# Kernel tuning notes

Measured on AMD Instinct MI355X. Metric: run time of the kernel, lower is better.

Reference implementation:

```python
import jax, jax.numpy as jnp
import numpy as np

EMBED_DIM = 1152
NUM_HEADS = 16
HEAD_DIM = EMBED_DIM // NUM_HEADS  # 72
TOTAL_TOKENS = 4096


def setup_inputs() -> dict:
    key = jax.random.key(0)
    k_x, k_wqkv, k_bqkv, k_wout, k_bout = jax.random.split(key, 5)
    hidden_states = jax.random.normal(k_x, (1, TOTAL_TOKENS, EMBED_DIM), dtype=jnp.float32)
    # fused QKV projection (use_qkv_parallel=True): weight [3*E, E], bias [3*E]
    w_qkv = jax.random.normal(k_wqkv, (3 * EMBED_DIM, EMBED_DIM), dtype=jnp.float32) * 0.02
    b_qkv = jax.random.normal(k_bqkv, (3 * EMBED_DIM,), dtype=jnp.float32) * 0.02
    # output projection [E, E]
    w_out = jax.random.normal(k_wout, (EMBED_DIM, EMBED_DIM), dtype=jnp.float32) * 0.02
    b_out = jax.random.normal(k_bout, (EMBED_DIM,), dtype=jnp.float32) * 0.02
    # 8 ragged sequences packed to 4096 tokens total
    cu_seqlens = jnp.array([0, 300, 900, 1500, 2124, 2600, 3100, 3624, 4096], dtype=jnp.int32)
    return {
        "hidden_states": hidden_states,
        "w_qkv": w_qkv,
        "b_qkv": b_qkv,
        "w_out": w_out,
        "b_out": b_out,
        "cu_seqlens": cu_seqlens,
        "max_seqlen": 1024,
    }


def _varlen_attention(x, w_qkv, b_qkv, w_out, b_out, cu_seqlens):
    # x: [T, E] packed tokens
    T = x.shape[0]
    qkv = x @ w_qkv.T + b_qkv                         # [T, 3E]
    q, k, v = jnp.split(qkv, 3, axis=-1)
    q = q.reshape(T, NUM_HEADS, HEAD_DIM)
    k = k.reshape(T, NUM_HEADS, HEAD_DIM)
    v = v.reshape(T, NUM_HEADS, HEAD_DIM)
    scale = HEAD_DIM ** -0.5
    # block-diagonal (per-sequence) attention via segment-id mask
    seg = jnp.searchsorted(cu_seqlens[1:], jnp.arange(T, dtype=jnp.int32), side="right")
    same_seq = seg[:, None] == seg[None, :]           # [T, T] bool
    scores = jnp.einsum("thd,shd->hts", q, k) * scale  # [H, T, T]
    scores = jnp.where(same_seq[None, :, :], scores, jnp.float32(-1e30))
    attn = jax.nn.softmax(scores, axis=-1)
    out = jnp.einsum("hts,shd->thd", attn, v).reshape(T, EMBED_DIM)
    return out @ w_out.T + b_out                      # [T, E]


def reference(hidden_states, w_qkv, b_qkv, w_out, b_out, cu_seqlens, max_seqlen):
    # max_seqlen is unused by the module (VisionAttention computes internally)
    out = _varlen_attention(hidden_states[0], w_qkv, b_qkv, w_out, b_out, cu_seqlens)
    return out[None]  # (1, total_tokens, embed_dim)
```

## Files before the change

### kernel.cpp

```cpp
#include <hip/hip_runtime.h>
#include <hip/hip_bf16.h>
#include <stdint.h>

typedef __hip_bfloat16 bf16;
typedef __attribute__((ext_vector_type(8))) short short8;
typedef __attribute__((ext_vector_type(4))) float float4v;

#define MFMA16(a, b, c) __builtin_amdgcn_mfma_f32_16x16x32_bf16((a), (b), (c), 0, 0, 0)

static __device__ __forceinline__ short f2bf(float f) {
    bf16 h = __float2bfloat16(f);
    return *reinterpret_cast<short*>(&h);
}

static __device__ __forceinline__ void gl2lds16(const void* g, void* l) {
    __builtin_amdgcn_global_load_lds(
        (const __attribute__((address_space(1))) void*)g,
        (__attribute__((address_space(3))) void*)l, 16, 0, 0);
}

__global__ __launch_bounds__(256) void cvt_all(
    const float* __restrict__ a, bf16* __restrict__ A, int na,
    const float* __restrict__ b, bf16* __restrict__ B, int nb,
    const float* __restrict__ c, bf16* __restrict__ C, int nc,
    float* __restrict__ z, int nz)
{
    int i = (blockIdx.x * 256 + threadIdx.x) * 8;
    const float* src; bf16* dst;
    if (i < na)                 { src = a; dst = A; }
    else if (i < na + nb)       { i -= na; src = b; dst = B; }
    else if (i < na + nb + nc)  { i -= na + nb; src = c; dst = C; }
    else {
        i -= na + nb + nc;
        if (i < nz) {
            const float4v zf = {0.f, 0.f, 0.f, 0.f};
            *(float4v*)(z + i) = zf;
            *(float4v*)(z + i + 4) = zf;
        }
        return;
    }
    const float4v x0 = *(const float4v*)(src + i);
    const float4v x1 = *(const float4v*)(src + i + 4);
    short8 v;
#pragma unroll
    for (int q = 0; q < 4; ++q) { v[q] = f2bf(x0[q]); v[q + 4] = f2bf(x1[q]); }
    *(short8*)(dst + i) = v;
}

__global__ __launch_bounds__(256) void gemm_xwt(
    const bf16* __restrict__ X, const bf16* __restrict__ W,
    const float* __restrict__ bias,
    float* __restrict__ Cout,
    bf16* __restrict__ Qh, bf16* __restrict__ Kh, bf16* __restrict__ Vt,
    int M, int N, int K, int mode)
{
    __shared__ __align__(16) bf16 SMEM[16384];
    bf16* As = SMEM;
    bf16* Bs = SMEM + 8192;

    const int tid  = threadIdx.x;
    const int wave = tid >> 6;
    const int lane = tid & 63;
    const int quad = lane >> 4;
    const int l16  = lane & 15;
    const int m0 = blockIdx.x * 128;
    const int n0 = blockIdx.y * 128;
    const int wm = (wave >> 1) * 64;
    const int wn = (wave & 1) * 64;

    const int lrow   = lane >> 2;
    const int lchunk = lane & 3;

    const int kper = K / gridDim.z;
    const int kbeg = blockIdx.z * kper;
    const int nIt  = kper >> 5;

    float4v acc[4][4];
    const float4v zf = {0.f, 0.f, 0.f, 0.f};
#pragma unroll
    for (int i = 0; i < 4; ++i)
#pragma unroll
        for (int j = 0; j < 4; ++j) acc[i][j] = zf;

    auto stage = [&](int buf, int k0) {
#pragma unroll
        for (int ii = 0; ii < 2; ++ii) {
            const int rbase = wave * 32 + ii * 16;
            const int r  = rbase + lrow;
            const int sc = lchunk ^ ((r >> 1) & 3);
            gl2lds16(&X[(size_t)(m0 + r) * K + k0 + sc * 8], &As[buf * 4096 + rbase * 32]);
            gl2lds16(&W[(size_t)(n0 + r) * K + k0 + sc * 8], &Bs[buf * 4096 + rbase * 32]);
        }
    };

    stage(0, kbeg);

    for (int it = 0; it < nIt; ++it) {
        __syncthreads();
        if (it + 1 < nIt) stage((it + 1) & 1, kbeg + (it + 1) * 32);

        const int b = it & 1;
        short8 af[4], bfr[4];
#pragma unroll
        for (int i = 0; i < 4; ++i) {
            const int r = wm + i * 16 + l16;
            af[i] = *(const short8*)&As[b * 4096 + r * 32 + (quad ^ ((r >> 1) & 3)) * 8];
        }
#pragma unroll
        for (int j = 0; j < 4; ++j) {
            const int r = wn + j * 16 + l16;
            bfr[j] = *(const short8*)&Bs[b * 4096 + r * 32 + (quad ^ ((r >> 1) & 3)) * 8];
        }
#pragma unroll
        for (int i = 0; i < 4; ++i)
#pragma unroll
            for (int j = 0; j < 4; ++j)
                acc[i][j] = MFMA16(af[i], bfr[j], acc[i][j]);
    }

    if (mode == 1 && n0 >= 2304) {
        bf16* T = SMEM;
#pragma unroll 1
        for (int half = 0; half < 2; ++half) {
            __syncthreads();
            if ((wave & 1) == half) {
#pragma unroll
                for (int j = 0; j < 4; ++j) {
                    const int col = n0 + wn + j * 16 + l16;
                    const float bb = bias[col];
#pragma unroll
                    for (int i = 0; i < 4; ++i)
#pragma unroll
                        for (int r = 0; r < 4; ++r)
                            T[(j * 16 + l16) * 136 + wm + i * 16 + quad * 4 + r] =
                                __float2bfloat16(acc[i][j][r] + bb);
                }
            }
            __syncthreads();
            const int dd   = tid >> 2;
            const int tok0 = (tid & 3) * 32;
            const int colg = n0 + half * 64 + dd - 2304;
            const int hh   = colg / 72;
            const int dm   = colg - hh * 72;
            bf16* dst = &Vt[((size_t)hh * 72 + dm) * 4096 + m0 + tok0];
#pragma unroll
            for (int k = 0; k < 4; ++k)
                *(short8*)(dst + k * 8) = *(const short8*)&T[dd * 136 + tok0 + k * 8];
        }
        return;
    }

    const bool split = (gridDim.z > 1);
    const float bscale = (!split || blockIdx.z == 0) ? 1.f : 0.f;
#pragma unroll
    for (int j = 0; j < 4; ++j) {
        const int col = n0 + wn + j * 16 + l16;
        const float bb = bias[col] * bscale;
#pragma unroll
        for (int i = 0; i < 4; ++i) {
#pragma unroll
            for (int r = 0; r < 4; ++r) {
                const int row = m0 + wm + i * 16 + quad * 4 + r;
                const float val = acc[i][j][r] + bb;
                if (mode == 0) {
                    if (split) atomicAdd(&Cout[(size_t)row * N + col], val);
                    else       Cout[(size_t)row * N + col] = val;
                } else {
                    const bf16 bv = __float2bfloat16(val);
                    if (col < 1152) {
                        const int hh = col / 72, dd = col - hh * 72;
                        Qh[((size_t)hh * 4096 + row) * 72 + dd] = bv;
                    } else {
                        const int c2 = col - 1152;
                        const int hh = c2 / 72, dd = c2 - hh * 72;
                        Kh[((size_t)hh * 4096 + row) * 72 + dd] = bv;
                    }
                }
            }
        }
    }
}

__global__ __launch_bounds__(256) void attn_varlen(
    const bf16* __restrict__ Qh, const bf16* __restrict__ Kh,
    const bf16* __restrict__ Vt,
    const int* __restrict__ cu, bf16* __restrict__ AO)
{
    const float scale = 0.11785113019775793f;
    __shared__ __align__(16) bf16 Ks[2][64 * 72];
    __shared__ __align__(16) bf16 Vs[2][80 * 64];
    __shared__ __align__(16) bf16 Ps[4][16 * 72];

    const int tid  = threadIdx.x;
    const int wave = tid >> 6;
    const int lane = tid & 63;
    const int quad = lane >> 4;
    const int l16  = lane & 15;
    const int h  = blockIdx.x & 15;
    const int qb = blockIdx.x >> 4;

    int seq_end = 0, q0 = -1, accb = 0, seq_start = 0;
    for (int i = 0; i < 8; ++i) {
        const int st = cu[i], en = cu[i + 1];
        const int nb = (en - st + 63) >> 6;
        if (q0 < 0 && qb < accb + nb) {
            seq_start = st; seq_end = en; q0 = st + (qb - accb) * 64;
        }
        accb += nb;
    }
    if (q0 < 0) return;

    const bf16 onev  = __float2bfloat16(1.0f);
    const bf16 zerov = __float2bfloat16(0.0f);
    for (int t = tid; t < 1024; t += 256) {
        const int b = t >> 9, rr = (t >> 6) & 7, cc = t & 63;
        Vs[b][(72 + rr) * 64 + cc] = (rr == 0) ? onev : zerov;
    }

    const short8 z8 = {0, 0, 0, 0, 0, 0, 0, 0};

    int qrow_f = q0 + wave * 16 + l16; if (qrow_f > 4095) qrow_f = 4095;
    const bf16* qp = &Qh[((size_t)h * 4096 + qrow_f) * 72];
    short8 aq[3];
    aq[0] = *(const short8*)(qp + quad * 8);
    aq[1] = *(const short8*)(qp + 32 + quad * 8);
    aq[2] = (quad == 0) ? *(const short8*)(qp + 64) : z8;

    const bf16* kbase = &Kh[(size_t)h * 4096 * 72];
    auto stage = [&](int buf, int kv0) {
        const bf16* ksrc = kbase + (size_t)kv0 * 72;
        for (int i = wave; i < 9; i += 4)
            gl2lds16(ksrc + i * 512 + lane * 8, &Ks[buf][i * 512]);
        for (int i = wave; i < 9; i += 4) {
            const int d  = i * 8 + (lane >> 3);
            const int ch = (lane & 7) ^ (d & 7);
            gl2lds16(&Vt[((size_t)h * 72 + d) * 4096 + kv0 + ch * 8],
                     &Vs[buf][i * 512]);
        }
    };

    const float4v zf = {0.f, 0.f, 0.f, 0.f};
    float4v oacc[5];
#pragma unroll
    for (int d = 0; d < 5; ++d) oacc[d] = zf;

    const int kvbeg = seq_start & ~63;
    stage(0, kvbeg);

    for (int kv0 = kvbeg; kv0 < seq_end; kv0 += 64) {
        const int b = ((kv0 - kvbeg) >> 6) & 1;
        __syncthreads();
        if (kv0 + 64 < seq_end) stage(b ^ 1, kv0 + 64);

        float4v sc[4];
#pragma unroll
        for (int nt = 0; nt < 4; ++nt) {
            const bf16* kb = &Ks[b][(nt * 16 + l16) * 72];
            float4v s = zf;
            s = MFMA16(aq[0], *(const short8*)(kb + quad * 8), s);
            s = MFMA16(aq[1], *(const short8*)(kb + 32 + quad * 8), s);
            s = MFMA16(aq[2], (quad == 0) ? *(const short8*)(kb + 64) : z8, s);
            sc[nt] = s;
        }

#pragma unroll
        for (int nt = 0; nt < 4; ++nt) {
            const int kv = kv0 + nt * 16 + l16;
            const bool ok = (kv >= seq_start) && (kv < seq_end);
#pragma unroll
            for (int r = 0; r < 4; ++r) {
                const float p = ok ? __expf(sc[nt][r] * scale) : 0.f;
                Ps[wave][(quad * 4 + r) * 72 + nt * 16 + l16] = __float2bfloat16(p);
            }
        }

        const short8 ap0 = *(const short8*)&Ps[wave][l16 * 72 + quad * 8];
        const short8 ap1 = *(const short8*)&Ps[wave][l16 * 72 + 32 + quad * 8];

#pragma unroll
        for (int dt = 0; dt < 5; ++dt) {
            const int vr = dt * 16 + l16;
            const bf16* vb = &Vs[b][vr * 64];
            const short8 bv0 = *(const short8*)(vb + ((quad ^ (vr & 7)) * 8));
            const short8 bv1 = *(const short8*)(vb + (((quad + 4) ^ (vr & 7)) * 8));
            oacc[dt] = MFMA16(ap0, bv0, oacc[dt]);
            oacc[dt] = MFMA16(ap1, bv1, oacc[dt]);
        }
    }

#pragma unroll
    for (int r = 0; r < 4; ++r) {
        const int qrow = q0 + wave * 16 + quad * 4 + r;
        const float lv = __shfl(oacc[4][r], (lane & 48) | 8);
        if (qrow < seq_end) {
            const float inv = (lv > 0.f) ? (1.0f / lv) : 0.f;
#pragma unroll
            for (int d = 0; d < 5; ++d) {
                const int dim = d * 16 + l16;
                if (dim < 72)
                    AO[(size_t)qrow * 1152 + h * 72 + dim] =
                        __float2bfloat16(oacc[d][r] * inv);
            }
        }
    }
}

extern "C" void kernel_launch(void* const* d_in, const int* in_sizes, int n_in,
                              void* d_out, int out_size, void* d_ws, size_t ws_size,
                              hipStream_t stream)
{
    const float* Xf   = (const float*)d_in[0];
    const float* Wqkv = (const float*)d_in[1];
    const float* Bqkv = (const float*)d_in[2];
    const float* Wout = (const float*)d_in[3];
    const float* Bout = (const float*)d_in[4];
    const int*   cu   = (const int*)d_in[5];

    const size_t X16_B  = (size_t)4096 * 1152 * 2;
    const size_t WQ16_B = (size_t)3456 * 1152 * 2;
    const size_t WO16_B = (size_t)1152 * 1152 * 2;
    const size_t H_B    = (size_t)16 * 4096 * 72 * 2;

    char* ws = (char*)d_ws;
    bf16* X16  = (bf16*)ws;
    bf16* WQ16 = (bf16*)(ws + X16_B);
    bf16* WO16 = (bf16*)(ws + X16_B + WQ16_B);
    bf16* Qh   = (bf16*)(ws + X16_B + WQ16_B + WO16_B);
    bf16* Kh   = (bf16*)(ws + X16_B + WQ16_B + WO16_B + H_B);
    bf16* Vt   = (bf16*)(ws + X16_B + WQ16_B + WO16_B + 2 * H_B);
    bf16* AO   = (bf16*)(ws + X16_B + WQ16_B + WO16_B + 3 * H_B);
    float* Out = (float*)d_out;

    dim3 blk(256);
    cvt_all<<<dim3(7200), blk, 0, stream>>>(Xf, X16, 4096 * 1152,
                                            Wqkv, WQ16, 3456 * 1152,
                                            Wout, WO16, 1152 * 1152,
                                            Out, 4096 * 1152);

    gemm_xwt<<<dim3(32, 27, 1), blk, 0, stream>>>(X16, WQ16, Bqkv, nullptr,
                                                  Qh, Kh, Vt, 4096, 3456, 1152, 1);
    attn_varlen<<<dim3(72 * 16), blk, 0, stream>>>(Qh, Kh, Vt, cu, AO);
    gemm_xwt<<<dim3(32, 9, 2), blk, 0, stream>>>(AO, WO16, Bout, Out,
                                                 nullptr, nullptr, nullptr,
                                                 4096, 1152, 1152, 0);
}
```

Before: 231.4 us.

## Drop split-K atomics and output zeroing; stage Q/K epilogue through LDS

The output projection no longer uses split-K with fp32 atomicAdd into a pre-zeroed buffer. It now runs as a dedicated 128x64-tile GEMM that writes results directly, so the conversion kernel no longer has to zero the output. The Q/K epilogue of the QKV GEMM now goes through LDS and writes coalesced 16-byte vectors into the per-head layouts instead of scattered 2-byte stores. These changes cut atomic traffic, a full-size memset and uncoalesced writes, at the cost of an extra LDS round trip and more blocks per output-GEMM tile.

```diff
diff --git a/kernel.cpp b/kernel.cpp
--- a/kernel.cpp
+++ b/kernel.cpp
@@ -22,23 +22,13 @@
 __global__ __launch_bounds__(256) void cvt_all(
     const float* __restrict__ a, bf16* __restrict__ A, int na,
     const float* __restrict__ b, bf16* __restrict__ B, int nb,
-    const float* __restrict__ c, bf16* __restrict__ C, int nc,
-    float* __restrict__ z, int nz)
+    const float* __restrict__ c, bf16* __restrict__ C, int nc)
 {
     int i = (blockIdx.x * 256 + threadIdx.x) * 8;
     const float* src; bf16* dst;
     if (i < na)                 { src = a; dst = A; }
     else if (i < na + nb)       { i -= na; src = b; dst = B; }
-    else if (i < na + nb + nc)  { i -= na + nb; src = c; dst = C; }
-    else {
-        i -= na + nb + nc;
-        if (i < nz) {
-            const float4v zf = {0.f, 0.f, 0.f, 0.f};
-            *(float4v*)(z + i) = zf;
-            *(float4v*)(z + i + 4) = zf;
-        }
-        return;
-    }
+    else                        { i -= na + nb; src = c; dst = C; if (i >= nc) return; }
     const float4v x0 = *(const float4v*)(src + i);
     const float4v x1 = *(const float4v*)(src + i + 4);
     short8 v;
@@ -47,12 +37,11 @@
     *(short8*)(dst + i) = v;
 }
 
-__global__ __launch_bounds__(256) void gemm_xwt(
+__global__ __launch_bounds__(256) void gemm_qkv(
     const bf16* __restrict__ X, const bf16* __restrict__ W,
     const float* __restrict__ bias,
-    float* __restrict__ Cout,
     bf16* __restrict__ Qh, bf16* __restrict__ Kh, bf16* __restrict__ Vt,
-    int M, int N, int K, int mode)
+    int M, int K)
 {
     __shared__ __align__(16) bf16 SMEM[16384];
     bf16* As = SMEM;
@@ -71,9 +60,7 @@
     const int lrow   = lane >> 2;
     const int lchunk = lane & 3;
 
-    const int kper = K / gridDim.z;
-    const int kbeg = blockIdx.z * kper;
-    const int nIt  = kper >> 5;
+    const int nIt = K >> 5;
 
     float4v acc[4][4];
     const float4v zf = {0.f, 0.f, 0.f, 0.f};
@@ -93,11 +80,11 @@
         }
     };
 
-    stage(0, kbeg);
+    stage(0, 0);
 
     for (int it = 0; it < nIt; ++it) {
         __syncthreads();
-        if (it + 1 < nIt) stage((it + 1) & 1, kbeg + (it + 1) * 32);
+        if (it + 1 < nIt) stage((it + 1) & 1, (it + 1) * 32);
 
         const int b = it & 1;
         short8 af[4], bfr[4];
@@ -118,8 +105,9 @@
                 acc[i][j] = MFMA16(af[i], bfr[j], acc[i][j]);
     }
 
-    if (mode == 1 && n0 >= 2304) {
-        bf16* T = SMEM;
+    bf16* T = SMEM;
+
+    if (n0 >= 2304) {
 #pragma unroll 1
         for (int half = 0; half < 2; ++half) {
             __syncthreads();
@@ -150,32 +138,120 @@
         return;
     }
 
-    const bool split = (gridDim.z > 1);
-    const float bscale = (!split || blockIdx.z == 0) ? 1.f : 0.f;
-#pragma unroll
-    for (int j = 0; j < 4; ++j) {
+#pragma unroll 1
+    for (int half = 0; half < 2; ++half) {
+        __syncthreads();
+        if ((wave >> 1) == half) {
+#pragma unroll
+            for (int j = 0; j < 4; ++j) {
+                const int col = n0 + wn + j * 16 + l16;
+                const float bb = bias[col];
+#pragma unroll
+                for (int i = 0; i < 4; ++i)
+#pragma unroll
+                    for (int r = 0; r < 4; ++r)
+                        T[(i * 16 + quad * 4 + r) * 136 + wn + j * 16 + l16] =
+                            __float2bfloat16(acc[i][j][r] + bb);
+            }
+        }
+        __syncthreads();
+        const int rloc = tid >> 2;
+        const int row  = m0 + half * 64 + rloc;
+        const int c0   = (tid & 3) * 32;
+#pragma unroll
+        for (int k = 0; k < 4; ++k) {
+            const int colg = n0 + c0 + k * 8;
+            const bool isQ = (colg < 1152);
+            const int cc = isQ ? colg : colg - 1152;
+            const int hh = cc / 72;
+            const int dd = cc - hh * 72;
+            bf16* dst = (isQ ? Qh : Kh) + ((size_t)hh * 4096 + row) * 72 + dd;
+            *(short8*)dst = *(const short8*)&T[rloc * 136 + c0 + k * 8];
+        }
+    }
+}
+
+__global__ __launch_bounds__(256) void gemm_out(
+    const bf16* __restrict__ X, const bf16* __restrict__ W,
+    const float* __restrict__ bias, float* __restrict__ Cout,
+    int M, int N, int K)
+{
+    __shared__ __align__(16) bf16 As[2][128 * 32];
+    __shared__ __align__(16) bf16 Bs[2][64 * 32];
+
+    const int tid  = threadIdx.x;
+    const int wave = tid >> 6;
+    const int lane = tid & 63;
+    const int quad = lane >> 4;
+    const int l16  = lane & 15;
+    const int m0 = blockIdx.x * 128;
+    const int n0 = blockIdx.y * 64;
+    const int wm = (wave >> 1) * 64;
+    const int wn = (wave & 1) * 32;
+
+    const int lrow   = lane >> 2;
+    const int lchunk = lane & 3;
+
+    const int nIt = K >> 5;
+
+    float4v acc[4][2];
+    const float4v zf = {0.f, 0.f, 0.f, 0.f};
+#pragma unroll
+    for (int i = 0; i < 4; ++i)
+#pragma unroll
+        for (int j = 0; j < 2; ++j) acc[i][j] = zf;
+
+    auto stage = [&](int buf, int k0) {
+#pragma unroll
+        for (int ii = 0; ii < 2; ++ii) {
+            const int rbase = wave * 32 + ii * 16;
+            const int r  = rbase + lrow;
+            const int sc = lchunk ^ ((r >> 1) & 3);
+            gl2lds16(&X[(size_t)(m0 + r) * K + k0 + sc * 8], &As[buf][rbase * 32]);
+        }
+        {
+            const int rbase = wave * 16;
+            const int r  = rbase + lrow;
+            const int sc = lchunk ^ ((r >> 1) & 3);
+            gl2lds16(&W[(size_t)(n0 + r) * K + k0 + sc * 8], &Bs[buf][rbase * 32]);
+        }
+    };
+
+    stage(0, 0);
+
+    for (int it = 0; it < nIt; ++it) {
+        __syncthreads();
+        if (it + 1 < nIt) stage((it + 1) & 1, (it + 1) * 32);
+
+        const int b = it & 1;
+        short8 af[4], bfr[2];
+#pragma unroll
+        for (int i = 0; i < 4; ++i) {
+            const int r = wm + i * 16 + l16;
+            af[i] = *(const short8*)&As[b][r * 32 + (quad ^ ((r >> 1) & 3)) * 8];
+        }
+#pragma unroll
+        for (int j = 0; j < 2; ++j) {
+            const int r = wn + j * 16 + l16;
+            bfr[j] = *(const short8*)&Bs[b][r * 32 + (quad ^ ((r >> 1) & 3)) * 8];
+        }
+#pragma unroll
+        for (int i = 0; i < 4; ++i)
+#pragma unroll
+            for (int j = 0; j < 2; ++j)
+                acc[i][j] = MFMA16(af[i], bfr[j], acc[i][j]);
+    }
+
+#pragma unroll
+    for (int j = 0; j < 2; ++j) {
         const int col = n0 + wn + j * 16 + l16;
-        const float bb = bias[col] * bscale;
+        const float bb = bias[col];
 #pragma unroll
         for (int i = 0; i < 4; ++i) {
 #pragma unroll
             for (int r = 0; r < 4; ++r) {
                 const int row = m0 + wm + i * 16 + quad * 4 + r;
-                const float val = acc[i][j][r] + bb;
-                if (mode == 0) {
-                    if (split) atomicAdd(&Cout[(size_t)row * N + col], val);
-                    else       Cout[(size_t)row * N + col] = val;
-                } else {
-                    const bf16 bv = __float2bfloat16(val);
-                    if (col < 1152) {
-                        const int hh = col / 72, dd = col - hh * 72;
-                        Qh[((size_t)hh * 4096 + row) * 72 + dd] = bv;
-                    } else {
-                        const int c2 = col - 1152;
-                        const int hh = c2 / 72, dd = c2 - hh * 72;
-                        Kh[((size_t)hh * 4096 + row) * 72 + dd] = bv;
-                    }
-                }
+                Cout[(size_t)row * N + col] = acc[i][j][r] + bb;
             }
         }
     }
@@ -332,15 +408,13 @@
     float* Out = (float*)d_out;
 
     dim3 blk(256);
-    cvt_all<<<dim3(7200), blk, 0, stream>>>(Xf, X16, 4096 * 1152,
+    cvt_all<<<dim3(4896), blk, 0, stream>>>(Xf, X16, 4096 * 1152,
                                             Wqkv, WQ16, 3456 * 1152,
-                                            Wout, WO16, 1152 * 1152,
-                                            Out, 4096 * 1152);
-
-    gemm_xwt<<<dim3(32, 27, 1), blk, 0, stream>>>(X16, WQ16, Bqkv, nullptr,
-                                                  Qh, Kh, Vt, 4096, 3456, 1152, 1);
+                                            Wout, WO16, 1152 * 1152);
+
+    gemm_qkv<<<dim3(32, 27), blk, 0, stream>>>(X16, WQ16, Bqkv,
+                                               Qh, Kh, Vt, 4096, 1152);
     attn_varlen<<<dim3(72 * 16), blk, 0, stream>>>(Qh, Kh, Vt, cu, AO);
-    gemm_xwt<<<dim3(32, 9, 2), blk, 0, stream>>>(AO, WO16, Bout, Out,
-                                                 nullptr, nullptr, nullptr,
-                                                 4096, 1152, 1152, 0);
-}
+    gemm_out<<<dim3(32, 18), blk, 0, stream>>>(AO, WO16, Bout, Out,
+                                               4096, 1152, 1152);
+}
```

New measurement: 202.9 us. 1.14x faster.
